# Performance work log

Hardware: AMD Instinct MI355X
Metric: run time of the kernel (lower is better)

Reference implementation:

```python
import jax, jax.numpy as jnp
import numpy as np

B, S, K = 64, 80, 32          # patients, max visits, codes per visit
V, E, H, L = 10000, 256, 512, 128  # vocab, embed, hidden, latent


def setup_inputs() -> dict:
    key = jax.random.key(0)
    ks = jax.random.split(key, 9)
    input_sequence = jax.random.randint(ks[0], (B, S, K), 0, V)
    length = jax.random.randint(ks[1], (B,), 1, S + 1)  # valid lengths >= 1
    sc = 0.05
    embedding_weight = jax.random.normal(ks[2], (V, E), jnp.float32) * sc
    Wi = jax.random.normal(ks[3], (3 * H, E), jnp.float32) * sc   # W_ih (r,z,n)
    Wh = jax.random.normal(ks[4], (3 * H, H), jnp.float32) * sc   # W_hh (r,z,n)
    bi = jax.random.normal(ks[5], (3 * H,), jnp.float32) * sc
    bh = jax.random.normal(ks[6], (3 * H,), jnp.float32) * sc
    W_lat = jax.random.normal(ks[7], (L, H), jnp.float32) * sc
    b_lat = jax.random.normal(ks[8], (L,), jnp.float32) * sc
    return dict(input_sequence=input_sequence, length=length,
                embedding_weight=embedding_weight, Wi=Wi, Wh=Wh, bi=bi, bh=bh,
                W_lat=W_lat, b_lat=b_lat)


def _encode(input_sequence, length, embedding_weight, Wi, Wh, bi, bh, W_lat, b_lat):
    b, s, k = input_sequence.shape
    v, e = embedding_weight.shape
    h = Wh.shape[1]
    # torch.sort(length, descending=True) -> batch reorder (output stays sorted!)
    sorted_idx = jnp.argsort(-length)
    sorted_len = length[sorted_idx]
    seq = input_sequence[sorted_idx]
    # multi-hot scatter: duplicates collapse to 1, matching torch scatter_(dim=2, val=1)
    onehot = jnp.zeros((b, s, v), jnp.float32)
    onehot = onehot.at[jnp.arange(b)[:, None, None],
                       jnp.arange(s)[None, :, None], seq].set(1.0)
    onehot = onehot.at[:, :, 0].set(0.0)  # code 0 is padding
    emb = jnp.tanh(jnp.einsum('bsv,ve->bse', onehot, embedding_weight))  # [B,S,E]
    # packed GRU == masked scan: hidden frozen once t >= length
    mask = jnp.arange(s)[None, :] < sorted_len[:, None]  # [B,S]
    xs = jnp.swapaxes(emb, 0, 1)   # [S,B,E]
    ms = jnp.swapaxes(mask, 0, 1)  # [S,B]

    def step(hprev, xm):
        x, m = xm
        gi = x @ Wi.T + bi        # [B,3H]
        gh = hprev @ Wh.T + bh    # [B,3H]
        i_r, i_z, i_n = jnp.split(gi, 3, axis=-1)
        h_r, h_z, h_n = jnp.split(gh, 3, axis=-1)
        r = jax.nn.sigmoid(i_r + h_r)
        z = jax.nn.sigmoid(i_z + h_z)
        n = jnp.tanh(i_n + r * h_n)
        hnew = (1.0 - z) * n + z * hprev
        return jnp.where(m[:, None], hnew, hprev), None

    h0 = jnp.zeros((b, h), jnp.float32)
    hT, _ = jax.lax.scan(step, h0, (xs, ms))  # last valid hidden per sequence
    return jnp.tanh(hT @ W_lat.T + b_lat)     # [B,L], in sorted order


def reference(input_sequence, length, embedding_weight, Wi, Wh, bi, bh, W_lat, b_lat):
    return _encode(input_sequence, length, embedding_weight, Wi, Wh, bi, bh, W_lat, b_lat)
```

## Files before the change

### kernel.cpp

```cpp
#include <hip/hip_runtime.h>
#include <cmath>

typedef _Float16 f16;
typedef _Float16 f16x8 __attribute__((ext_vector_type(8)));
typedef float f32x4 __attribute__((ext_vector_type(4)));
typedef unsigned int u32x4 __attribute__((ext_vector_type(4)));

#define B 64
#define S 80
#define KC 32
#define EDIM 256
#define HDIM 512
#define G3 1536
#define LDIM 128

#define NG 8
#define PG 8
#define NJ 32
#define CPB 16

#define OFF_PCNT  (NG * NJ * 64)
#define OFF_XCD   (OFF_PCNT + NG * 64)
#define OFF_TEST  (OFF_XCD + NG * NJ)
#define OFF_FAIL  (OFF_TEST + NG * NJ * 64)
#define SYNC_TOTAL (OFF_FAIL + NG)

__device__ __forceinline__ unsigned int ld_u32c(const unsigned int* p, bool l2) {
    unsigned int v;
    if (l2) {
        asm volatile("global_load_dword %0, %1, off sc0\n\ts_waitcnt vmcnt(0)"
                     : "=v"(v) : "v"(p) : "memory");
    } else {
        v = __hip_atomic_load(p, __ATOMIC_RELAXED, __HIP_MEMORY_SCOPE_AGENT);
    }
    return v;
}
__device__ __forceinline__ void st_u32c(unsigned int* p, unsigned int v, bool l2) {
    if (l2) {
        asm volatile("global_store_dword %0, %1, off sc0" :: "v"(p), "v"(v) : "memory");
    } else {
        __hip_atomic_store(p, v, __ATOMIC_RELAXED, __HIP_MEMORY_SCOPE_AGENT);
    }
}

__global__ __launch_bounds__(256) void emb_kernel(const int* __restrict__ seq,
                                                  const float* __restrict__ Ew,
                                                  unsigned short* __restrict__ emb16) {
    int bs = blockIdx.x;
    __shared__ int codes[KC];
    __shared__ int valid[KC];
    int tid = threadIdx.x;
    if (tid < KC) codes[tid] = seq[bs * KC + tid];
    __syncthreads();
    if (tid < KC) {
        int c = codes[tid];
        int v = (c != 0);
        for (int i = 0; i < tid; ++i)
            if (codes[i] == c) v = 0;
        valid[tid] = v;
    }
    __syncthreads();
    float acc = 0.f;
    for (int j = 0; j < KC; ++j) {
        if (valid[j]) acc += Ew[codes[j] * EDIM + tid];
    }
    emb16[bs * EDIM + tid] = __builtin_bit_cast(unsigned short, (f16)tanhf(acc));
}

__global__ __launch_bounds__(256) void gi_gemm16(
        const unsigned short* __restrict__ wi16,
        const unsigned short* __restrict__ emb16,
        const float* __restrict__ bi,
        unsigned short* __restrict__ gi16) {
    __shared__ __align__(16) f16 At[64][256];
    __shared__ __align__(16) f16 Bt[64][256];
    const int m0 = blockIdx.x * 64;
    const int n0 = blockIdx.y * 64;
    const int tid = threadIdx.x;
    #pragma unroll
    for (int i = 0; i < 8; ++i) {
        int ci = tid + i * 256;
        int row = ci >> 5, c = ci & 31;
        int sc = c ^ (row & 7);
        *(f32x4*)&At[row][sc * 8] =
            *(const f32x4*)(wi16 + (size_t)(n0 + row) * EDIM + c * 8);
        *(f32x4*)&Bt[row][sc * 8] =
            *(const f32x4*)(emb16 + (size_t)(m0 + row) * EDIM + c * 8);
    }
    __syncthreads();
    const int wv = tid >> 6, ln = tid & 63;
    const int lr = ln & 15, hi = ln >> 4;
    const int arow = wv * 16 + lr;
    f32x4 acc[4] = {};
    #pragma unroll
    for (int ks = 0; ks < 8; ++ks) {
        int ca = (ks * 4 + hi) ^ (arow & 7);
        f32x4 av = *(const f32x4*)&At[arow][ca * 8];
        #pragma unroll
        for (int vt = 0; vt < 4; ++vt) {
            int brow = vt * 16 + lr;
            int cb = (ks * 4 + hi) ^ (brow & 7);
            f32x4 bv = *(const f32x4*)&Bt[brow][cb * 8];
            acc[vt] = __builtin_amdgcn_mfma_f32_16x16x32_f16(
                __builtin_bit_cast(f16x8, av), __builtin_bit_cast(f16x8, bv),
                acc[vt], 0, 0, 0);
        }
    }
    const int gate0 = n0 + wv * 16 + hi * 4;
    float4 bv4 = *(const float4*)(bi + gate0);
    #pragma unroll
    for (int vt = 0; vt < 4; ++vt) {
        int vis = m0 + vt * 16 + lr;
        union { unsigned short u[4]; unsigned long long ll; } pk;
        pk.u[0] = __builtin_bit_cast(unsigned short, (f16)(acc[vt][0] + bv4.x));
        pk.u[1] = __builtin_bit_cast(unsigned short, (f16)(acc[vt][1] + bv4.y));
        pk.u[2] = __builtin_bit_cast(unsigned short, (f16)(acc[vt][2] + bv4.z));
        pk.u[3] = __builtin_bit_cast(unsigned short, (f16)(acc[vt][3] + bv4.w));
        *(unsigned long long*)(gi16 + (size_t)vis * G3 + gate0) = pk.ll;
    }
}

__global__ __launch_bounds__(256) void init_kernel(const int* __restrict__ len,
                                                   const float* __restrict__ Wi,
                                                   const float* __restrict__ Wh,
                                                   int* __restrict__ rank,
                                                   unsigned int* __restrict__ sync,
                                                   unsigned int* __restrict__ hz,
                                                   unsigned short* __restrict__ wi16,
                                                   unsigned short* __restrict__ wh16) {
    int idx = blockIdx.x * 256 + threadIdx.x;
    if (idx < 16384) { hz[idx] = 0u; hz[16384 + idx] = 0u; }
    for (int o = idx; o < SYNC_TOTAL; o += 32768) sync[o] = 0u;
    for (int o = idx; o < G3 * EDIM; o += 32768)
        wi16[o] = __builtin_bit_cast(unsigned short, (f16)Wi[o]);
    for (int o = idx; o < G3 * HDIM; o += 32768)
        wh16[o] = __builtin_bit_cast(unsigned short, (f16)Wh[o]);
    if (blockIdx.x == 0 && threadIdx.x < B) {
        int t = threadIdx.x;
        int lb = len[t];
        int r = 0;
        for (int i = 0; i < B; ++i) {
            int li = len[i];
            r += (li > lb) || (li == lb && i < t);
        }
        rank[t] = r;
    }
}

__global__ __launch_bounds__(256, 1) void gru_persist(
        const unsigned short* __restrict__ gi16,
        const unsigned short* __restrict__ wh16,
        const float* __restrict__ bh, const int* __restrict__ len,
        unsigned short* __restrict__ h0f, unsigned short* __restrict__ h1f,
        unsigned short* __restrict__ hout,
        unsigned int* __restrict__ sync) {
    const int g     = blockIdx.x;
    const int slice = blockIdx.y;
    const int tid   = threadIdx.x;
    const int wv    = tid >> 6;
    const int ln    = tid & 63;
    const int c0    = slice * CPB;

    __shared__ __align__(16) f16 hsb[64][16][8];
    __shared__ float ghl[3][16][16];
    __shared__ f16 hst[PG][CPB];
    __shared__ unsigned int ids_sh[NJ];
    __shared__ unsigned int fail_sh;

    for (int c = tid; c < 64 * 8; c += 256)
        *(float4*)&hsb[c >> 3][8 + (c & 7)][0] = make_float4(0.f, 0.f, 0.f, 0.f);

    f32x4 af[16];
    if (wv < 3) {
        const unsigned short* wrow =
            wh16 + (size_t)(wv * HDIM + c0 + (ln & 15)) * HDIM + (ln >> 4) * 8;
        #pragma unroll
        for (int ks = 0; ks < 16; ++ks)
            af[ks] = *(const f32x4*)(wrow + ks * 32);
    } else {
        #pragma unroll
        for (int ks = 0; ks < 16; ++ks) af[ks] = (f32x4){0.f, 0.f, 0.f, 0.f};
    }
    #pragma unroll
    for (int ks = 0; ks < 16; ++ks) asm volatile("" : "+v"(af[ks]));

    unsigned int* gflags = sync + (size_t)(g * NJ) * 64;
    unsigned int* pcnt   = sync + OFF_PCNT + g * 64;
    unsigned int* xcdrow = sync + OFF_XCD + g * NJ;
    unsigned int* town   = sync + OFF_TEST + (g * NJ + slice) * 64;
    unsigned int* tpeer  = sync + OFF_TEST + (g * NJ + ((slice + 1) & (NJ - 1))) * 64;
    unsigned int* failw  = sync + OFF_FAIL + g;

    auto l3bar = [&](unsigned int target) {
        if (tid == 0) {
            asm volatile("s_waitcnt vmcnt(0)" ::: "memory");
            __hip_atomic_fetch_add(pcnt, 1u, __ATOMIC_RELAXED, __HIP_MEMORY_SCOPE_AGENT);
            while (__hip_atomic_load(pcnt, __ATOMIC_RELAXED, __HIP_MEMORY_SCOPE_AGENT) < target)
                __builtin_amdgcn_s_sleep(1);
        }
        __syncthreads();
    };

    unsigned int myxcc;
    asm volatile("s_getreg_b32 %0, hwreg(HW_REG_XCC_ID)" : "=s"(myxcc));
    myxcc &= 0xFu;
    if (tid == 0)
        __hip_atomic_store(xcdrow + slice, myxcc, __ATOMIC_RELAXED, __HIP_MEMORY_SCOPE_AGENT);
    l3bar(NJ);
    if (tid < NJ)
        ids_sh[tid] = __hip_atomic_load(xcdrow + tid, __ATOMIC_RELAXED, __HIP_MEMORY_SCOPE_AGENT);
    __syncthreads();
    bool same_xcd = true;
    #pragma unroll
    for (int i = 1; i < NJ; ++i) same_xcd &= (ids_sh[i] == ids_sh[0]);

    bool l2m = false;
    if (same_xcd) {
        const unsigned int M1 = 0xA5A50000u + (unsigned)slice;
        const unsigned int M2 = 0x5A5A0000u + (unsigned)slice;
        const unsigned int P1 = 0xA5A50000u + (unsigned)((slice + 1) & (NJ - 1));
        const unsigned int P2 = 0x5A5A0000u + (unsigned)((slice + 1) & (NJ - 1));
        unsigned int r1 = 0, r2 = 0;
        if (tid == 0) st_u32c(town, M1, true);
        l3bar(2 * NJ);
        if (tid == 0) r1 = ld_u32c(tpeer, true);
        l3bar(3 * NJ);
        if (tid == 0) st_u32c(town, M2, true);
        l3bar(4 * NJ);
        if (tid == 0) {
            r2 = ld_u32c(tpeer, true);
            if (r1 != P1 || r2 != P2)
                __hip_atomic_fetch_or(failw, 1u, __ATOMIC_RELAXED, __HIP_MEMORY_SCOPE_AGENT);
        }
        l3bar(5 * NJ);
        if (tid == 0)
            fail_sh = __hip_atomic_load(failw, __ATOMIC_RELAXED, __HIP_MEMORY_SCOPE_AGENT);
        __syncthreads();
        l2m = (fail_sh == 0u);
    }

    const int pat  = tid & 7;
    const int hc   = tid >> 3;
    const int colg = c0 + hc;
    const int fb   = g * PG + pat;
    float bhr = 0.f, bhz = 0.f, bhn = 0.f;
    const unsigned short* gi_b = gi16;
    int flen = 0;
    if (tid < 128) {
        bhr = bh[colg]; bhz = bh[HDIM + colg]; bhn = bh[2 * HDIM + colg];
        gi_b = gi16 + (size_t)fb * S * G3;
        flen = len[fb];
    }
    int Lg = 0;
    #pragma unroll
    for (int i = 0; i < PG; ++i) Lg = max(Lg, len[g * PG + i]);

    unsigned short* hb0 = h0f + (size_t)g * PG * HDIM;
    unsigned short* hb1 = h1f + (size_t)g * PG * HDIM;

    const int g0p = tid & 7,         g0k = tid >> 3;
    const int g1p = g0p,             g1k = g0k + 32;

    float gr = 0.f, gz = 0.f, gn = 0.f;
    if (tid < 128) {
        gr = (float)__builtin_bit_cast(f16, gi_b[colg]);
        gz = (float)__builtin_bit_cast(f16, gi_b[HDIM + colg]);
        gn = (float)__builtin_bit_cast(f16, gi_b[2 * HDIM + colg]);
    }

    float lastH = 0.f;

    #pragma unroll 1
    for (int t = 0; t < Lg; ++t) {
        const unsigned short* src = (t & 1) ? hb1 : hb0;
        unsigned short*       dst = (t & 1) ? hb0 : hb1;

        {
            const unsigned short* p0 = src + g0p * HDIM + g0k * 8;
            const unsigned short* p1 = src + g1p * HDIM + g1k * 8;
            if (l2m) {
                u32x4 v0, v1;
                asm volatile(
                    "global_load_dwordx4 %0, %2, off sc0\n\t"
                    "global_load_dwordx4 %1, %3, off sc0\n\t"
                    "s_waitcnt vmcnt(0)"
                    : "=v"(v0), "=v"(v1) : "v"(p0), "v"(p1) : "memory");
                *(u32x4*)&hsb[g0k][g0p][0] = v0;
                *(u32x4*)&hsb[g1k][g1p][0] = v1;
            } else {
                u32x4 v0, v1;
                #pragma unroll
                for (int i = 0; i < 4; ++i) {
                    v0[i] = __hip_atomic_load((const unsigned int*)p0 + i,
                                              __ATOMIC_RELAXED, __HIP_MEMORY_SCOPE_AGENT);
                    v1[i] = __hip_atomic_load((const unsigned int*)p1 + i,
                                              __ATOMIC_RELAXED, __HIP_MEMORY_SCOPE_AGENT);
                }
                *(u32x4*)&hsb[g0k][g0p][0] = v0;
                *(u32x4*)&hsb[g1k][g1p][0] = v1;
            }
        }
        __syncthreads();

        if (wv < 3) {
            f32x4 a0 = (f32x4){0.f, 0.f, 0.f, 0.f};
            f32x4 a1 = (f32x4){0.f, 0.f, 0.f, 0.f};
            #pragma unroll
            for (int ks = 0; ks < 8; ++ks) {
                f32x4 bv = *(const f32x4*)&hsb[ks * 4 + (ln >> 4)][ln & 15][0];
                a0 = __builtin_amdgcn_mfma_f32_16x16x32_f16(
                    __builtin_bit_cast(f16x8, af[ks]),
                    __builtin_bit_cast(f16x8, bv), a0, 0, 0, 0);
            }
            #pragma unroll
            for (int ks = 8; ks < 16; ++ks) {
                f32x4 bv = *(const f32x4*)&hsb[ks * 4 + (ln >> 4)][ln & 15][0];
                a1 = __builtin_amdgcn_mfma_f32_16x16x32_f16(
                    __builtin_bit_cast(f16x8, af[ks]),
                    __builtin_bit_cast(f16x8, bv), a1, 0, 0, 0);
            }
            #pragma unroll
            for (int i = 0; i < 4; ++i)
                ghl[wv][(ln >> 4) * 4 + i][ln & 15] = a0[i] + a1[i];
        }
        __syncthreads();

        if (tid < 128) {
            float sr = ghl[0][hc][pat], sz = ghl[1][hc][pat], sn = ghl[2][hc][pat];
            float r  = 1.f / (1.f + expf(-(gr + sr + bhr)));
            float z  = 1.f / (1.f + expf(-(gz + sz + bhz)));
            float nn = tanhf(gn + r * (sn + bhn));
            float hold = (float)hsb[colg >> 3][pat][colg & 7];
            float hnew = (t < flen) ? ((1.f - z) * nn + z * hold) : hold;
            lastH = hnew;
            hst[pat][hc] = (f16)hnew;
        }
        __syncthreads();

        if (tid < 64) {
            int sp = tid >> 3, dw = tid & 7;
            unsigned int v = *(const unsigned int*)&hst[sp][dw * 2];
            unsigned short* d = dst + sp * HDIM + c0 + dw * 2;
            if (l2m) {
                asm volatile("global_store_dword %0, %1, off sc0"
                             :: "v"(d), "v"(v) : "memory");
            } else {
                __hip_atomic_store((unsigned int*)d, v,
                                   __ATOMIC_RELAXED, __HIP_MEMORY_SCOPE_AGENT);
            }
        }
        asm volatile("s_waitcnt vmcnt(0)" ::: "memory");
        if (tid == 0) st_u32c(gflags + slice * 64, (unsigned)(t + 1), l2m);

        float nr = 0.f, nz = 0.f, nn2 = 0.f;
        if (tid < 128) {
            int tn = (t + 1 < S) ? (t + 1) : (S - 1);
            const unsigned short* gp = gi_b + (size_t)tn * G3;
            nr  = (float)__builtin_bit_cast(f16, gp[colg]);
            nz  = (float)__builtin_bit_cast(f16, gp[HDIM + colg]);
            nn2 = (float)__builtin_bit_cast(f16, gp[2 * HDIM + colg]);
        }

        if (tid < NJ) {
            unsigned int* f = gflags + tid * 64;
            while (ld_u32c(f, l2m) < (unsigned)(t + 1))
                __builtin_amdgcn_s_sleep(1);
        }
        __syncthreads();

        gr = nr; gz = nz; gn = nn2;
    }

    if (tid < 128)
        hout[(size_t)fb * HDIM + colg] = __builtin_bit_cast(unsigned short, (f16)lastH);
}

__global__ __launch_bounds__(128) void final_kernel(const unsigned short* __restrict__ h,
                                                    const float* __restrict__ Wl,
                                                    const float* __restrict__ bl,
                                                    const int* __restrict__ rank,
                                                    float* __restrict__ out) {
    int b = blockIdx.x;
    int l = threadIdx.x;
    __shared__ float hsh[HDIM];
    for (int i = l; i < HDIM; i += LDIM)
        hsh[i] = (float)__builtin_bit_cast(f16, h[(size_t)b * HDIM + i]);
    __syncthreads();
    float acc = bl[l];
    for (int k = 0; k < HDIM; ++k) acc += hsh[k] * Wl[(size_t)l * HDIM + k];
    out[(size_t)rank[b] * LDIM + l] = tanhf(acc);
}

extern "C" void kernel_launch(void* const* d_in, const int* in_sizes, int n_in,
                              void* d_out, int out_size, void* d_ws, size_t ws_size,
                              hipStream_t stream) {
    const int*   seq = (const int*)d_in[0];
    const int*   len = (const int*)d_in[1];
    const float* Ew  = (const float*)d_in[2];
    const float* Wi  = (const float*)d_in[3];
    const float* Wh  = (const float*)d_in[4];
    const float* bi  = (const float*)d_in[5];
    const float* bh  = (const float*)d_in[6];
    const float* Wl  = (const float*)d_in[7];
    const float* bl  = (const float*)d_in[8];
    float* out = (float*)d_out;

    unsigned short* ws16 = (unsigned short*)d_ws;
    unsigned short* emb16 = ws16;
    unsigned short* gi16  = emb16 + (size_t)B * S * EDIM;
    unsigned short* wi16  = gi16 + (size_t)B * S * G3;
    unsigned short* wh16  = wi16 + (size_t)G3 * EDIM;
    unsigned short* h0f   = wh16 + (size_t)G3 * HDIM;
    unsigned short* h1f   = h0f + (size_t)B * HDIM;
    unsigned short* hout  = h1f + (size_t)B * HDIM;
    int*   rank = (int*)(hout + (size_t)B * HDIM);
    unsigned int* sync = (unsigned int*)(rank + B);

    emb_kernel<<<B * S, 256, 0, stream>>>(seq, Ew, emb16);
    init_kernel<<<128, 256, 0, stream>>>(len, Wi, Wh, rank, sync,
                                         (unsigned int*)h0f, wi16, wh16);
    gi_gemm16<<<dim3(B * S / 64, G3 / 64), 256, 0, stream>>>(wi16, emb16, bi, gi16);

    gru_persist<<<dim3(NG, NJ), 256, 0, stream>>>(gi16, wh16, bh, len,
                                                  h0f, h1f, hout, sync);
    final_kernel<<<B, LDIM, 0, stream>>>(hout, Wl, bl, rank, out);
}
```

Measured before the change: 279.6 us.

## Widen GRU column slices to cut per-step grid barrier participants

Each persistent block now owns 64 hidden columns instead of 16, so each patient group needs 8 blocks instead of 32 and the per-step flag barrier polls fewer peers. Every wave now runs all three gate MFMAs for its own 16 columns and applies the gate nonlinearity directly on the accumulator registers, removing the shared-memory gate staging and two __syncthreads per step. The trade-off is three times more weight registers per thread (48 f32x4) and fewer blocks in flight, which raises register pressure and cuts parallelism. Half of the lanes, those whose MFMA output column is a padding patient, compute but take no part in the gate math.

```diff
diff --git a/kernel.cpp b/kernel.cpp
--- a/kernel.cpp
+++ b/kernel.cpp
@@ -2,8 +2,10 @@
 #include <cmath>
 
 typedef _Float16 f16;
+typedef _Float16 f16x4 __attribute__((ext_vector_type(4)));
 typedef _Float16 f16x8 __attribute__((ext_vector_type(8)));
 typedef float f32x4 __attribute__((ext_vector_type(4)));
+typedef unsigned int u32x2 __attribute__((ext_vector_type(2)));
 typedef unsigned int u32x4 __attribute__((ext_vector_type(4)));
 
 #define B 64
@@ -16,8 +18,8 @@
 
 #define NG 8
 #define PG 8
-#define NJ 32
-#define CPB 16
+#define NJ 8
+#define CPB 64
 
 #define OFF_PCNT  (NG * NJ * 64)
 #define OFF_XCD   (OFF_PCNT + NG * 64)
@@ -161,28 +163,28 @@
     const int ln    = tid & 63;
     const int c0    = slice * CPB;
 
-    __shared__ __align__(16) f16 hsb[64][16][8];
-    __shared__ float ghl[3][16][16];
-    __shared__ f16 hst[PG][CPB];
+    __shared__ __align__(16) f16 hsb[64][17][8];
     __shared__ unsigned int ids_sh[NJ];
     __shared__ unsigned int fail_sh;
 
     for (int c = tid; c < 64 * 8; c += 256)
         *(float4*)&hsb[c >> 3][8 + (c & 7)][0] = make_float4(0.f, 0.f, 0.f, 0.f);
 
-    f32x4 af[16];
-    if (wv < 3) {
+    const int pat   = ln & 15;
+    const int cq    = ln >> 4;
+    const int cbase = c0 + wv * 16 + cq * 4;
+    const bool act  = (pat < 8);
+    const int fb    = g * PG + (pat & 7);
+
+    f32x4 af[3][16];
+    #pragma unroll
+    for (int gg = 0; gg < 3; ++gg) {
         const unsigned short* wrow =
-            wh16 + (size_t)(wv * HDIM + c0 + (ln & 15)) * HDIM + (ln >> 4) * 8;
+            wh16 + (size_t)(gg * HDIM + c0 + wv * 16 + pat) * HDIM + cq * 8;
         #pragma unroll
         for (int ks = 0; ks < 16; ++ks)
-            af[ks] = *(const f32x4*)(wrow + ks * 32);
-    } else {
-        #pragma unroll
-        for (int ks = 0; ks < 16; ++ks) af[ks] = (f32x4){0.f, 0.f, 0.f, 0.f};
-    }
-    #pragma unroll
-    for (int ks = 0; ks < 16; ++ks) asm volatile("" : "+v"(af[ks]));
+            af[gg][ks] = *(const f32x4*)(wrow + ks * 32);
+    }
 
     unsigned int* gflags = sync + (size_t)(g * NJ) * 64;
     unsigned int* pcnt   = sync + OFF_PCNT + g * 64;
@@ -239,15 +241,13 @@
         l2m = (fail_sh == 0u);
     }
 
-    const int pat  = tid & 7;
-    const int hc   = tid >> 3;
-    const int colg = c0 + hc;
-    const int fb   = g * PG + pat;
-    float bhr = 0.f, bhz = 0.f, bhn = 0.f;
+    float4 bhv[3] = {};
     const unsigned short* gi_b = gi16;
     int flen = 0;
-    if (tid < 128) {
-        bhr = bh[colg]; bhz = bh[HDIM + colg]; bhn = bh[2 * HDIM + colg];
+    if (act) {
+        #pragma unroll
+        for (int gg = 0; gg < 3; ++gg)
+            bhv[gg] = *(const float4*)(bh + gg * HDIM + cbase);
         gi_b = gi16 + (size_t)fb * S * G3;
         flen = len[fb];
     }
@@ -258,26 +258,32 @@
     unsigned short* hb0 = h0f + (size_t)g * PG * HDIM;
     unsigned short* hb1 = h1f + (size_t)g * PG * HDIM;
 
-    const int g0p = tid & 7,         g0k = tid >> 3;
-    const int g1p = g0p,             g1k = g0k + 32;
-
-    float gr = 0.f, gz = 0.f, gn = 0.f;
-    if (tid < 128) {
-        gr = (float)__builtin_bit_cast(f16, gi_b[colg]);
-        gz = (float)__builtin_bit_cast(f16, gi_b[HDIM + colg]);
-        gn = (float)__builtin_bit_cast(f16, gi_b[2 * HDIM + colg]);
-    }
-
-    float lastH = 0.f;
+    const int g0p = tid & 7, g0k = tid >> 3;
+    const int g1k = g0k + 32;
+
+    f16x4 giC[3] = {};
+    if (act) {
+        #pragma unroll
+        for (int gg = 0; gg < 3; ++gg)
+            giC[gg] = *(const f16x4*)(gi_b + gg * HDIM + cbase);
+    }
+
+    f16x4 lastH = {};
 
     #pragma unroll 1
     for (int t = 0; t < Lg; ++t) {
+        #pragma unroll
+        for (int gg = 0; gg < 3; ++gg)
+            #pragma unroll
+            for (int ks = 0; ks < 16; ++ks)
+                asm volatile("" : "+v"(af[gg][ks]));
+
         const unsigned short* src = (t & 1) ? hb1 : hb0;
         unsigned short*       dst = (t & 1) ? hb0 : hb1;
 
         {
             const unsigned short* p0 = src + g0p * HDIM + g0k * 8;
-            const unsigned short* p1 = src + g1p * HDIM + g1k * 8;
+            const unsigned short* p1 = src + g0p * HDIM + g1k * 8;
             if (l2m) {
                 u32x4 v0, v1;
                 asm volatile(
@@ -286,7 +292,7 @@
                     "s_waitcnt vmcnt(0)"
                     : "=v"(v0), "=v"(v1) : "v"(p0), "v"(p1) : "memory");
                 *(u32x4*)&hsb[g0k][g0p][0] = v0;
-                *(u32x4*)&hsb[g1k][g1p][0] = v1;
+                *(u32x4*)&hsb[g1k][g0p][0] = v1;
             } else {
                 u32x4 v0, v1;
                 #pragma unroll
@@ -297,68 +303,82 @@
                                               __ATOMIC_RELAXED, __HIP_MEMORY_SCOPE_AGENT);
                 }
                 *(u32x4*)&hsb[g0k][g0p][0] = v0;
-                *(u32x4*)&hsb[g1k][g1p][0] = v1;
+                *(u32x4*)&hsb[g1k][g0p][0] = v1;
             }
         }
         __syncthreads();
 
-        if (wv < 3) {
-            f32x4 a0 = (f32x4){0.f, 0.f, 0.f, 0.f};
-            f32x4 a1 = (f32x4){0.f, 0.f, 0.f, 0.f};
+        f32x4 s0[3], s1[3];
+        #pragma unroll
+        for (int gg = 0; gg < 3; ++gg) {
+            s0[gg] = (f32x4){0.f, 0.f, 0.f, 0.f};
+            s1[gg] = (f32x4){0.f, 0.f, 0.f, 0.f};
+        }
+        #pragma unroll
+        for (int ks = 0; ks < 8; ++ks) {
+            f32x4 bv = *(const f32x4*)&hsb[ks * 4 + cq][pat][0];
             #pragma unroll
-            for (int ks = 0; ks < 8; ++ks) {
-                f32x4 bv = *(const f32x4*)&hsb[ks * 4 + (ln >> 4)][ln & 15][0];
-                a0 = __builtin_amdgcn_mfma_f32_16x16x32_f16(
-                    __builtin_bit_cast(f16x8, af[ks]),
-                    __builtin_bit_cast(f16x8, bv), a0, 0, 0, 0);
+            for (int gg = 0; gg < 3; ++gg)
+                s0[gg] = __builtin_amdgcn_mfma_f32_16x16x32_f16(
+                    __builtin_bit_cast(f16x8, af[gg][ks]),
+                    __builtin_bit_cast(f16x8, bv), s0[gg], 0, 0, 0);
+        }
+        #pragma unroll
+        for (int ks = 8; ks < 16; ++ks) {
+            f32x4 bv = *(const f32x4*)&hsb[ks * 4 + cq][pat][0];
+            #pragma unroll
+            for (int gg = 0; gg < 3; ++gg)
+                s1[gg] = __builtin_amdgcn_mfma_f32_16x16x32_f16(
+                    __builtin_bit_cast(f16x8, af[gg][ks]),
+                    __builtin_bit_cast(f16x8, bv), s1[gg], 0, 0, 0);
+        }
+
+        if (act) {
+            f16x4 holdv = *(const f16x4*)&hsb[cbase >> 3][pat][cbase & 7];
+            union { f16 h[4]; u32x2 v; } pk;
+            #pragma unroll
+            for (int i = 0; i < 4; ++i) {
+                float sr = s0[0][i] + s1[0][i];
+                float sz = s0[1][i] + s1[1][i];
+                float sn = s0[2][i] + s1[2][i];
+                float gr = (float)giC[0][i], gz = (float)giC[1][i],
+                      gn = (float)giC[2][i];
+                float bb = (i == 0) ? bhv[0].x : (i == 1) ? bhv[0].y
+                         : (i == 2) ? bhv[0].z : bhv[0].w;
+                float bz = (i == 0) ? bhv[1].x : (i == 1) ? bhv[1].y
+                         : (i == 2) ? bhv[1].z : bhv[1].w;
+                float bn = (i == 0) ? bhv[2].x : (i == 1) ? bhv[2].y
+                         : (i == 2) ? bhv[2].z : bhv[2].w;
+                float r  = 1.f / (1.f + expf(-(gr + sr + bb)));
+                float z  = 1.f / (1.f + expf(-(gz + sz + bz)));
+                float nn = tanhf(gn + r * (sn + bn));
+                float hold = (float)holdv[i];
+                float hnew = (t < flen) ? ((1.f - z) * nn + z * hold) : hold;
+                pk.h[i] = (f16)hnew;
             }
-            #pragma unroll
-            for (int ks = 8; ks < 16; ++ks) {
-                f32x4 bv = *(const f32x4*)&hsb[ks * 4 + (ln >> 4)][ln & 15][0];
-                a1 = __builtin_amdgcn_mfma_f32_16x16x32_f16(
-                    __builtin_bit_cast(f16x8, af[ks]),
-                    __builtin_bit_cast(f16x8, bv), a1, 0, 0, 0);
-            }
-            #pragma unroll
-            for (int i = 0; i < 4; ++i)
-                ghl[wv][(ln >> 4) * 4 + i][ln & 15] = a0[i] + a1[i];
-        }
-        __syncthreads();
-
-        if (tid < 128) {
-            float sr = ghl[0][hc][pat], sz = ghl[1][hc][pat], sn = ghl[2][hc][pat];
-            float r  = 1.f / (1.f + expf(-(gr + sr + bhr)));
-            float z  = 1.f / (1.f + expf(-(gz + sz + bhz)));
-            float nn = tanhf(gn + r * (sn + bhn));
-            float hold = (float)hsb[colg >> 3][pat][colg & 7];
-            float hnew = (t < flen) ? ((1.f - z) * nn + z * hold) : hold;
-            lastH = hnew;
-            hst[pat][hc] = (f16)hnew;
-        }
-        __syncthreads();
-
-        if (tid < 64) {
-            int sp = tid >> 3, dw = tid & 7;
-            unsigned int v = *(const unsigned int*)&hst[sp][dw * 2];
-            unsigned short* d = dst + sp * HDIM + c0 + dw * 2;
+            lastH = *(f16x4*)&pk.h[0];
+            unsigned short* d = dst + pat * HDIM + cbase;
             if (l2m) {
-                asm volatile("global_store_dword %0, %1, off sc0"
-                             :: "v"(d), "v"(v) : "memory");
+                asm volatile("global_store_dwordx2 %0, %1, off sc0"
+                             :: "v"(d), "v"(pk.v) : "memory");
             } else {
-                __hip_atomic_store((unsigned int*)d, v,
+                __hip_atomic_store((unsigned int*)d, pk.v[0],
+                                   __ATOMIC_RELAXED, __HIP_MEMORY_SCOPE_AGENT);
+                __hip_atomic_store((unsigned int*)d + 1, pk.v[1],
                                    __ATOMIC_RELAXED, __HIP_MEMORY_SCOPE_AGENT);
             }
         }
         asm volatile("s_waitcnt vmcnt(0)" ::: "memory");
+        __syncthreads();
         if (tid == 0) st_u32c(gflags + slice * 64, (unsigned)(t + 1), l2m);
 
-        float nr = 0.f, nz = 0.f, nn2 = 0.f;
-        if (tid < 128) {
+        f16x4 giN[3] = {};
+        if (act) {
             int tn = (t + 1 < S) ? (t + 1) : (S - 1);
             const unsigned short* gp = gi_b + (size_t)tn * G3;
-            nr  = (float)__builtin_bit_cast(f16, gp[colg]);
-            nz  = (float)__builtin_bit_cast(f16, gp[HDIM + colg]);
-            nn2 = (float)__builtin_bit_cast(f16, gp[2 * HDIM + colg]);
+            #pragma unroll
+            for (int gg = 0; gg < 3; ++gg)
+                giN[gg] = *(const f16x4*)(gp + gg * HDIM + cbase);
         }
 
         if (tid < NJ) {
@@ -368,11 +388,14 @@
         }
         __syncthreads();
 
-        gr = nr; gz = nz; gn = nn2;
-    }
-
-    if (tid < 128)
-        hout[(size_t)fb * HDIM + colg] = __builtin_bit_cast(unsigned short, (f16)lastH);
+        giC[0] = giN[0]; giC[1] = giN[1]; giC[2] = giN[2];
+    }
+
+    if (act) {
+        union { f16 h[4]; u32x2 v; } pk;
+        *(f16x4*)&pk.h[0] = lastH;
+        *(u32x2*)(hout + (size_t)fb * HDIM + cbase) = pk.v;
+    }
 }
 
 __global__ __launch_bounds__(128) void final_kernel(const unsigned short* __restrict__ h,
```

After: 340.5 us. +21.8%, slower.

## Halve GRU slice count per group, doubling columns per block with LDS-resident weights

Applied to the files above, without the earlier changes.

Reduces the number of cooperating blocks per patient group from 32 to 16, with each block now owning 32 hidden columns. Because the larger weight slice no longer fits in registers, it is staged once into padded LDS. Each wave runs two MFMA column tiles per gate, and the gate update handles two columns per thread, so the packed result is stored straight to global memory without the hst staging step. The intent is to cut the cross-block flag synchronisation fan-in per timestep and the total number of blocks. In exchange, each block does twice the MFMA work per step and reads its weights from LDS every step.

```diff
diff --git a/kernel.cpp b/kernel.cpp
--- a/kernel.cpp
+++ b/kernel.cpp
@@ -16,8 +16,8 @@
 
 #define NG 8
 #define PG 8
-#define NJ 32
-#define CPB 16
+#define NJ 16
+#define CPB 32
 
 #define OFF_PCNT  (NG * NJ * 64)
 #define OFF_XCD   (OFF_PCNT + NG * 64)
@@ -161,28 +161,23 @@
     const int ln    = tid & 63;
     const int c0    = slice * CPB;
 
+    __shared__ __align__(16) f32x4 wlds[96 * 65];
     __shared__ __align__(16) f16 hsb[64][16][8];
-    __shared__ float ghl[3][16][16];
-    __shared__ f16 hst[PG][CPB];
+    __shared__ float ghl[3][CPB][16];
     __shared__ unsigned int ids_sh[NJ];
     __shared__ unsigned int fail_sh;
 
     for (int c = tid; c < 64 * 8; c += 256)
         *(float4*)&hsb[c >> 3][8 + (c & 7)][0] = make_float4(0.f, 0.f, 0.f, 0.f);
 
-    f32x4 af[16];
-    if (wv < 3) {
-        const unsigned short* wrow =
-            wh16 + (size_t)(wv * HDIM + c0 + (ln & 15)) * HDIM + (ln >> 4) * 8;
-        #pragma unroll
-        for (int ks = 0; ks < 16; ++ks)
-            af[ks] = *(const f32x4*)(wrow + ks * 32);
-    } else {
-        #pragma unroll
-        for (int ks = 0; ks < 16; ++ks) af[ks] = (f32x4){0.f, 0.f, 0.f, 0.f};
-    }
-    #pragma unroll
-    for (int ks = 0; ks < 16; ++ks) asm volatile("" : "+v"(af[ks]));
+    #pragma unroll
+    for (int i = 0; i < 24; ++i) {
+        int idx = tid + i * 256;
+        int row = idx >> 6, slot = idx & 63;
+        int gate = row >> 5, lr = row & 31;
+        wlds[row * 65 + slot] =
+            *(const f32x4*)(wh16 + (size_t)(gate * HDIM + c0 + lr) * HDIM + slot * 8);
+    }
 
     unsigned int* gflags = sync + (size_t)(g * NJ) * 64;
     unsigned int* pcnt   = sync + OFF_PCNT + g * 64;
@@ -239,15 +234,18 @@
         l2m = (fail_sh == 0u);
     }
 
-    const int pat  = tid & 7;
-    const int hc   = tid >> 3;
-    const int colg = c0 + hc;
+    const int pat  = tid >> 4;
+    const int cp   = tid & 15;
+    const int colw = cp * 2;
+    const int colg = c0 + colw;
     const int fb   = g * PG + pat;
-    float bhr = 0.f, bhz = 0.f, bhn = 0.f;
+    float2 bhp[3] = {};
     const unsigned short* gi_b = gi16;
     int flen = 0;
     if (tid < 128) {
-        bhr = bh[colg]; bhz = bh[HDIM + colg]; bhn = bh[2 * HDIM + colg];
+        #pragma unroll
+        for (int gg = 0; gg < 3; ++gg)
+            bhp[gg] = *(const float2*)(bh + gg * HDIM + colg);
         gi_b = gi16 + (size_t)fb * S * G3;
         flen = len[fb];
     }
@@ -258,17 +256,17 @@
     unsigned short* hb0 = h0f + (size_t)g * PG * HDIM;
     unsigned short* hb1 = h1f + (size_t)g * PG * HDIM;
 
-    const int g0p = tid & 7,         g0k = tid >> 3;
-    const int g1p = g0p,             g1k = g0k + 32;
-
-    float gr = 0.f, gz = 0.f, gn = 0.f;
+    const int g0p = tid & 7, g0k = tid >> 3;
+    const int g1k = g0k + 32;
+
+    unsigned int giC[3] = {};
     if (tid < 128) {
-        gr = (float)__builtin_bit_cast(f16, gi_b[colg]);
-        gz = (float)__builtin_bit_cast(f16, gi_b[HDIM + colg]);
-        gn = (float)__builtin_bit_cast(f16, gi_b[2 * HDIM + colg]);
-    }
-
-    float lastH = 0.f;
+        #pragma unroll
+        for (int gg = 0; gg < 3; ++gg)
+            giC[gg] = *(const unsigned int*)(gi_b + gg * HDIM + colg);
+    }
+
+    unsigned int lastH = 0;
 
     #pragma unroll 1
     for (int t = 0; t < Lg; ++t) {
@@ -277,7 +275,7 @@
 
         {
             const unsigned short* p0 = src + g0p * HDIM + g0k * 8;
-            const unsigned short* p1 = src + g1p * HDIM + g1k * 8;
+            const unsigned short* p1 = src + g0p * HDIM + g1k * 8;
             if (l2m) {
                 u32x4 v0, v1;
                 asm volatile(
@@ -286,7 +284,7 @@
                     "s_waitcnt vmcnt(0)"
                     : "=v"(v0), "=v"(v1) : "v"(p0), "v"(p1) : "memory");
                 *(u32x4*)&hsb[g0k][g0p][0] = v0;
-                *(u32x4*)&hsb[g1k][g1p][0] = v1;
+                *(u32x4*)&hsb[g1k][g0p][0] = v1;
             } else {
                 u32x4 v0, v1;
                 #pragma unroll
@@ -297,68 +295,89 @@
                                               __ATOMIC_RELAXED, __HIP_MEMORY_SCOPE_AGENT);
                 }
                 *(u32x4*)&hsb[g0k][g0p][0] = v0;
-                *(u32x4*)&hsb[g1k][g1p][0] = v1;
+                *(u32x4*)&hsb[g1k][g0p][0] = v1;
             }
         }
         __syncthreads();
 
         if (wv < 3) {
-            f32x4 a0 = (f32x4){0.f, 0.f, 0.f, 0.f};
-            f32x4 a1 = (f32x4){0.f, 0.f, 0.f, 0.f};
+            const int lr = ln & 15, hi = ln >> 4;
             #pragma unroll
-            for (int ks = 0; ks < 8; ++ks) {
-                f32x4 bv = *(const f32x4*)&hsb[ks * 4 + (ln >> 4)][ln & 15][0];
-                a0 = __builtin_amdgcn_mfma_f32_16x16x32_f16(
-                    __builtin_bit_cast(f16x8, af[ks]),
-                    __builtin_bit_cast(f16x8, bv), a0, 0, 0, 0);
+            for (int cc = 0; cc < 2; ++cc) {
+                const f32x4* wrow = &wlds[(wv * 32 + cc * 16 + lr) * 65 + hi];
+                f32x4 a0 = (f32x4){0.f, 0.f, 0.f, 0.f};
+                f32x4 a1 = (f32x4){0.f, 0.f, 0.f, 0.f};
+                #pragma unroll
+                for (int ks = 0; ks < 8; ++ks) {
+                    f32x4 av = wrow[ks * 4];
+                    f32x4 bv = *(const f32x4*)&hsb[ks * 4 + hi][lr][0];
+                    a0 = __builtin_amdgcn_mfma_f32_16x16x32_f16(
+                        __builtin_bit_cast(f16x8, av),
+                        __builtin_bit_cast(f16x8, bv), a0, 0, 0, 0);
+                }
+                #pragma unroll
+                for (int ks = 8; ks < 16; ++ks) {
+                    f32x4 av = wrow[ks * 4];
+                    f32x4 bv = *(const f32x4*)&hsb[ks * 4 + hi][lr][0];
+                    a1 = __builtin_amdgcn_mfma_f32_16x16x32_f16(
+                        __builtin_bit_cast(f16x8, av),
+                        __builtin_bit_cast(f16x8, bv), a1, 0, 0, 0);
+                }
+                #pragma unroll
+                for (int i = 0; i < 4; ++i)
+                    ghl[wv][cc * 16 + hi * 4 + i][lr] = a0[i] + a1[i];
             }
+        }
+        __syncthreads();
+
+        if (tid < 128) {
+            unsigned int hold2 =
+                *(const unsigned int*)&hsb[colg >> 3][pat][colg & 7];
+            union { f16 h[2]; unsigned int v; } pk, hv;
+            hv.v = hold2;
             #pragma unroll
-            for (int ks = 8; ks < 16; ++ks) {
-                f32x4 bv = *(const f32x4*)&hsb[ks * 4 + (ln >> 4)][ln & 15][0];
-                a1 = __builtin_amdgcn_mfma_f32_16x16x32_f16(
-                    __builtin_bit_cast(f16x8, af[ks]),
-                    __builtin_bit_cast(f16x8, bv), a1, 0, 0, 0);
+            for (int i = 0; i < 2; ++i) {
+                float sr = ghl[0][colw + i][pat];
+                float sz = ghl[1][colw + i][pat];
+                float sn = ghl[2][colw + i][pat];
+                f16 g2[2];
+                *(unsigned int*)g2 = giC[0];
+                float gr = (float)g2[i];
+                *(unsigned int*)g2 = giC[1];
+                float gz = (float)g2[i];
+                *(unsigned int*)g2 = giC[2];
+                float gn = (float)g2[i];
+                float bb = i ? bhp[0].y : bhp[0].x;
+                float bz = i ? bhp[1].y : bhp[1].x;
+                float bn = i ? bhp[2].y : bhp[2].x;
+                float r  = 1.f / (1.f + expf(-(gr + sr + bb)));
+                float z  = 1.f / (1.f + expf(-(gz + sz + bz)));
+                float nn = tanhf(gn + r * (sn + bn));
+                float hold = (float)hv.h[i];
+                float hnew = (t < flen) ? ((1.f - z) * nn + z * hold) : hold;
+                pk.h[i] = (f16)hnew;
             }
-            #pragma unroll
-            for (int i = 0; i < 4; ++i)
-                ghl[wv][(ln >> 4) * 4 + i][ln & 15] = a0[i] + a1[i];
-        }
-        __syncthreads();
-
-        if (tid < 128) {
-            float sr = ghl[0][hc][pat], sz = ghl[1][hc][pat], sn = ghl[2][hc][pat];
-            float r  = 1.f / (1.f + expf(-(gr + sr + bhr)));
-            float z  = 1.f / (1.f + expf(-(gz + sz + bhz)));
-            float nn = tanhf(gn + r * (sn + bhn));
-            float hold = (float)hsb[colg >> 3][pat][colg & 7];
-            float hnew = (t < flen) ? ((1.f - z) * nn + z * hold) : hold;
-            lastH = hnew;
-            hst[pat][hc] = (f16)hnew;
-        }
-        __syncthreads();
-
-        if (tid < 64) {
-            int sp = tid >> 3, dw = tid & 7;
-            unsigned int v = *(const unsigned int*)&hst[sp][dw * 2];
-            unsigned short* d = dst + sp * HDIM + c0 + dw * 2;
+            lastH = pk.v;
+            unsigned short* d = dst + pat * HDIM + colg;
             if (l2m) {
                 asm volatile("global_store_dword %0, %1, off sc0"
-                             :: "v"(d), "v"(v) : "memory");
+                             :: "v"(d), "v"(pk.v) : "memory");
             } else {
-                __hip_atomic_store((unsigned int*)d, v,
+                __hip_atomic_store((unsigned int*)d, pk.v,
                                    __ATOMIC_RELAXED, __HIP_MEMORY_SCOPE_AGENT);
             }
         }
         asm volatile("s_waitcnt vmcnt(0)" ::: "memory");
+        __syncthreads();
         if (tid == 0) st_u32c(gflags + slice * 64, (unsigned)(t + 1), l2m);
 
-        float nr = 0.f, nz = 0.f, nn2 = 0.f;
+        unsigned int giN[3] = {};
         if (tid < 128) {
             int tn = (t + 1 < S) ? (t + 1) : (S - 1);
             const unsigned short* gp = gi_b + (size_t)tn * G3;
-            nr  = (float)__builtin_bit_cast(f16, gp[colg]);
-            nz  = (float)__builtin_bit_cast(f16, gp[HDIM + colg]);
-            nn2 = (float)__builtin_bit_cast(f16, gp[2 * HDIM + colg]);
+            #pragma unroll
+            for (int gg = 0; gg < 3; ++gg)
+                giN[gg] = *(const unsigned int*)(gp + gg * HDIM + colg);
         }
 
         if (tid < NJ) {
@@ -368,11 +387,11 @@
         }
         __syncthreads();
 
-        gr = nr; gz = nz; gn = nn2;
+        giC[0] = giN[0]; giC[1] = giN[1]; giC[2] = giN[2];
     }
 
     if (tid < 128)
-        hout[(size_t)fb * HDIM + colg] = __builtin_bit_cast(unsigned short, (f16)lastH);
+        *(unsigned int*)(hout + (size_t)fb * HDIM + colg) = lastH;
 }
 
 __global__ __launch_bounds__(128) void final_kernel(const unsigned short* __restrict__ h,
```

New measurement: 323.2 us. +15.6%, slower.
